# Kernel tuning notes

Measured on AMD Instinct MI355X. Metric: run time of the kernel, lower is better.

Reference implementation:

```python
import jax, jax.numpy as jnp
import numpy as np

B, T, D, E, TOP_K = 4, 4096, 1024, 8, 2
CAPACITY_FACTOR = 1.5


def setup_inputs() -> dict:
    key = jax.random.key(0)
    k1, k2, k3 = jax.random.split(key, 3)
    x = jax.random.normal(k1, (B, T, D), dtype=jnp.float32)
    Wr = jax.random.normal(k2, (E, D), dtype=jnp.float32) * 0.02   # router weight [E, D]
    We = jax.random.normal(k3, (E, D, D), dtype=jnp.float32) * 0.02  # per-expert dense [E, D, D]
    return {"x": x, "Wr": Wr, "We": We}


def reference(x, Wr, We):
    Bb, Tt, Dd = x.shape
    Ee = Wr.shape[0]
    K = TOP_K
    C = int(Tt * K / Ee * CAPACITY_FACTOR) + 1  # max_tokens_per_expert

    # Router + fused top-k softmax (triton_topk_softmax semantics)
    logits = jnp.einsum('btd,ed->bte', x, Wr)                 # [B, T, E]
    top_vals, top_idx = jax.lax.top_k(logits, K)              # [B, T, K]
    w = jax.nn.softmax(top_vals, axis=-1)                     # [B, T, K]

    # Position of each (token, k) slot inside its expert's capacity buffer,
    # assigned in (t, k) order -- matches the sequential counter in _build_position_map.
    flat_e = top_idx.reshape(Bb, Tt * K)                      # [B, T*K]
    oh = jax.nn.one_hot(flat_e, Ee, dtype=jnp.int32)          # [B, T*K, E]
    pos_all = jnp.cumsum(oh, axis=1) - oh                     # count of earlier slots per expert
    pos = jnp.take_along_axis(pos_all, flat_e[..., None], axis=-1)[..., 0]  # [B, T*K]
    keep = pos < C                                            # capacity drop

    # Scatter tokens into [B, E, C, D] capacity buffers (triton_expert_scatter)
    b_idx = jnp.arange(Bb, dtype=jnp.int32)[:, None]
    dst = (b_idx * Ee + flat_e) * C + pos                     # flat buffer index
    dst = jnp.where(keep, dst, Bb * Ee * C).reshape(-1)       # out-of-range -> dropped
    x_rep = jnp.repeat(x, K, axis=1).reshape(-1, Dd)          # [B*T*K, D]
    buf = jnp.zeros((Bb * Ee * C, Dd), dtype=x.dtype).at[dst].add(x_rep, mode='drop')
    expert_in = buf.reshape(Bb, Ee, C, Dd)

    # expert_fn: per-expert dense layer (grouped GEMM)
    expert_out = jnp.einsum('becd,edf->becf', expert_in, We)  # [B, E, C, D]

    # Gather back + weighted combine (triton_expert_gather)
    gathered = jnp.take(expert_out.reshape(Bb * Ee * C, Dd), dst, axis=0,
                        mode='fill', fill_value=0.0)          # dropped slots -> 0
    gathered = gathered.reshape(Bb, Tt, K, Dd)
    out = jnp.einsum('btk,btkd->btd', w, gathered)            # [B, T, D]
    return out
```

## Files before the change

kernel.cpp:

```cpp
#include <hip/hip_runtime.h>
#include <hip/hip_bf16.h>
#include <math.h>

#define B_ 4
#define T_ 4096
#define D_ 1024
#define E_ 8
#define K_ 2
#define C_ 1537

typedef short bf16x8 __attribute__((ext_vector_type(8)));
typedef float f32x4 __attribute__((ext_vector_type(4)));

__device__ __forceinline__ unsigned short f2bf(float f) {
    union { float f; unsigned int u; } c; c.f = f;
    unsigned int u = c.u;
    unsigned int r = (u + 0x7fffu + ((u >> 16) & 1u)) >> 16;
    return (unsigned short)r;
}

__device__ __forceinline__ void gl2lds16(const unsigned short* g, unsigned short* l) {
    __builtin_amdgcn_global_load_lds(
        (const __attribute__((address_space(1))) unsigned int*)g,
        (__attribute__((address_space(3))) unsigned int*)l, 16, 0, 0);
}

__global__ __launch_bounds__(256) void router_kernel(
    const float* __restrict__ x, const float* __restrict__ Wr,
    unsigned short* __restrict__ xbf, int* __restrict__ top_e,
    float* __restrict__ wbuf) {
    __shared__ float wr_s[E_ * D_];
    int tid = threadIdx.x;
    const float4* wr4 = (const float4*)Wr;
    float4* wrs4 = (float4*)wr_s;
    for (int i = tid; i < E_ * D_ / 4; i += 256) wrs4[i] = wr4[i];
    __syncthreads();

    int wave = tid >> 6, lane = tid & 63;
    int token = blockIdx.x * 4 + wave;

    const float4* xr = (const float4*)(x + (size_t)token * D_) + lane * 4;
    float xs[16];
    #pragma unroll
    for (int i = 0; i < 4; i++) {
        float4 v = xr[i];
        xs[i * 4 + 0] = v.x; xs[i * 4 + 1] = v.y;
        xs[i * 4 + 2] = v.z; xs[i * 4 + 3] = v.w;
    }

    unsigned short xb[16];
    #pragma unroll
    for (int i = 0; i < 16; i++) xb[i] = f2bf(xs[i]);
    uint4* dst = (uint4*)(xbf + (size_t)token * D_ + lane * 16);
    dst[0] = ((uint4*)xb)[0];
    dst[1] = ((uint4*)xb)[1];

    double acc[E_];
    #pragma unroll
    for (int e = 0; e < E_; e++) {
        const float* wp = wr_s + e * D_ + lane * 16;
        double a = 0.0;
        #pragma unroll
        for (int i = 0; i < 16; i++) a += (double)xs[i] * (double)wp[i];
        acc[e] = a;
    }
    #pragma unroll
    for (int e = 0; e < E_; e++) {
        #pragma unroll
        for (int off = 32; off > 0; off >>= 1)
            acc[e] += __shfl_down(acc[e], off, 64);
    }

    if (lane == 0) {
        int e0 = 0; double v0 = acc[0];
        #pragma unroll
        for (int e = 1; e < E_; e++) if (acc[e] > v0) { v0 = acc[e]; e0 = e; }
        int e1 = -1; double v1 = -1.0e300;
        #pragma unroll
        for (int e = 0; e < E_; e++) if (e != e0 && acc[e] > v1) { v1 = acc[e]; e1 = e; }
        double ex = exp(v1 - v0);
        float w0 = (float)(1.0 / (1.0 + ex));
        float w1 = (float)(ex / (1.0 + ex));
        top_e[token * 2 + 0] = e0;
        top_e[token * 2 + 1] = e1;
        wbuf[token * 2 + 0] = w0;
        wbuf[token * 2 + 1] = w1;
    }
}

__global__ __launch_bounds__(256) void wt_kernel(const float* __restrict__ We,
                                                 unsigned short* __restrict__ wtbf) {
    __shared__ unsigned short tile[64][65];
    int e = blockIdx.x >> 8;
    int t = blockIdx.x & 255;
    int d0 = (t >> 4) * 64, f0 = (t & 15) * 64;
    const float* src = We + ((size_t)e * D_ + d0) * D_ + f0;
    int tid = threadIdx.x;
    #pragma unroll
    for (int i = 0; i < 4; i++) {
        int idx = tid + i * 256;
        int r = idx >> 4, c4 = (idx & 15) * 4;
        float4 v = *(const float4*)(src + (size_t)r * D_ + c4);
        tile[r][c4 + 0] = f2bf(v.x); tile[r][c4 + 1] = f2bf(v.y);
        tile[r][c4 + 2] = f2bf(v.z); tile[r][c4 + 3] = f2bf(v.w);
    }
    __syncthreads();
    unsigned short* dstp = wtbf + ((size_t)e * D_ + f0) * D_ + d0;
    int r = tid >> 2, c0 = (tid & 3) * 16;
    unsigned short vals[16];
    #pragma unroll
    for (int j = 0; j < 16; j++) vals[j] = tile[c0 + j][r];
    *(uint4*)(dstp + (size_t)r * D_ + c0)     = ((const uint4*)vals)[0];
    *(uint4*)(dstp + (size_t)r * D_ + c0 + 8) = ((const uint4*)vals)[1];
}

__global__ __launch_bounds__(256) void scan_kernel(const int* __restrict__ top_e,
                                                   int* __restrict__ list,
                                                   int* __restrict__ count) {
    int b = blockIdx.x, tid = threadIdx.x;
    const int S = T_ * K_;
    const int per = S / 256;
    __shared__ int cnt[256][E_];
    int local[E_];
    #pragma unroll
    for (int e = 0; e < E_; e++) local[e] = 0;
    const int* te = top_e + (size_t)b * S + tid * per;
    int evals[32];
    for (int i = 0; i < per; i++) { evals[i] = te[i]; local[evals[i]]++; }
    #pragma unroll
    for (int e = 0; e < E_; e++) cnt[tid][e] = local[e];
    __syncthreads();
    if (tid < E_) {
        int run = 0;
        for (int i = 0; i < 256; i++) { int v = cnt[i][tid]; cnt[i][tid] = run; run += v; }
        count[b * E_ + tid] = min(run, C_);
    }
    __syncthreads();
    int base[E_];
    #pragma unroll
    for (int e = 0; e < E_; e++) base[e] = cnt[tid][e];
    int* lst = list + (size_t)b * E_ * C_;
    for (int i = 0; i < per; i++) {
        int ev = evals[i];
        int p = base[ev]++;
        if (p < C_) lst[ev * C_ + p] = tid * per + i;
    }
}

__global__ __launch_bounds__(256) void gemm_kernel(
    const unsigned short* __restrict__ xbf, const unsigned short* __restrict__ wtbf,
    const int* __restrict__ list, const int* __restrict__ count,
    const float* __restrict__ wbuf, float* __restrict__ out) {
    int cb = blockIdx.x & 7;
    int rb = (blockIdx.x >> 3) % 13;
    int pe = blockIdx.x / 104;
    int b = pe >> 3, e = pe & 7;
    int cnt = count[pe];
    int row0 = rb * 128;
    if (row0 >= cnt) return;
    int rows = min(128, cnt - row0);

    __shared__ unsigned short As[2][128 * 32];
    __shared__ unsigned short Bs[2][128 * 32];
    __shared__ int slots[128];

    int tid = threadIdx.x;
    if (tid < 128) slots[tid] = (tid < rows) ? list[pe * C_ + row0 + tid] : 0;
    __syncthreads();

    int w = tid >> 6, l = tid & 63;
    int rA0 = w * 16 + (l >> 2);
    int rA1 = rA0 + 64;
    int ch  = l & 3;
    int cS0 = ch ^ ((rA0 >> 1) & 3);
    int cS1 = ch ^ ((rA1 >> 1) & 3);
    int tA0 = slots[rA0] >> 1, tA1 = slots[rA1] >> 1;
    const unsigned short* gA0 = xbf + ((size_t)b * T_ + tA0) * D_ + cS0 * 8;
    const unsigned short* gA1 = xbf + ((size_t)b * T_ + tA1) * D_ + cS1 * 8;
    const unsigned short* gB0 = wtbf + ((size_t)e * D_ + cb * 128 + rA0) * D_ + cS0 * 8;
    const unsigned short* gB1 = wtbf + ((size_t)e * D_ + cb * 128 + rA1) * D_ + cS1 * 8;
    int sOff = w * 512 + l * 8;

    int wave = w, lane = l;
    int wm = wave >> 1, wn = wave & 1;
    int quad = lane >> 4, mrow = lane & 15;
    int qe = quad ^ ((mrow >> 1) & 3);
    int aRd = wm * 2048 + mrow * 32 + qe * 8;
    int bRd = wn * 2048 + mrow * 32 + qe * 8;

    f32x4 acc[4][4];
    #pragma unroll
    for (int i = 0; i < 4; i++)
        #pragma unroll
        for (int j = 0; j < 4; j++) acc[i][j] = (f32x4){0.f, 0.f, 0.f, 0.f};

#define STAGE(buf, kk) do {                                   \
        unsigned short* sA = &As[buf][sOff];                  \
        unsigned short* sB = &Bs[buf][sOff];                  \
        gl2lds16(gA0 + (kk) * 32, sA);                        \
        gl2lds16(gA1 + (kk) * 32, sA + 2048);                 \
        gl2lds16(gB0 + (kk) * 32, sB);                        \
        gl2lds16(gB1 + (kk) * 32, sB + 2048);                 \
    } while (0)

    STAGE(0, 0);
    __syncthreads();
    int cur = 0;
    for (int kk = 0; kk < 32; kk++) {
        if (kk < 31) STAGE(cur ^ 1, kk + 1);
        bf16x8 af[4], bfv[4];
        #pragma unroll
        for (int i = 0; i < 4; i++)
            af[i] = *(const bf16x8*)(&As[cur][aRd + i * 512]);
        #pragma unroll
        for (int j = 0; j < 4; j++)
            bfv[j] = *(const bf16x8*)(&Bs[cur][bRd + j * 512]);
        #pragma unroll
        for (int i = 0; i < 4; i++)
            #pragma unroll
            for (int j = 0; j < 4; j++)
                acc[i][j] = __builtin_amdgcn_mfma_f32_16x16x32_bf16(af[i], bfv[j], acc[i][j], 0, 0, 0);
        __syncthreads();
        cur ^= 1;
    }
#undef STAGE

    float* outb = out + (size_t)b * T_ * D_;
    const float* wb = wbuf + (size_t)b * T_ * 2;
    int ncolbase = cb * 128 + wn * 64 + mrow;
    #pragma unroll
    for (int i = 0; i < 4; i++) {
        #pragma unroll
        for (int r = 0; r < 4; r++) {
            int m = wm * 64 + i * 16 + quad * 4 + r;
            if (m < rows) {
                int s = slots[m];
                int t = s >> 1;
                float wgt = wb[t * 2 + (s & 1)];
                float* orow = outb + (size_t)t * D_;
                #pragma unroll
                for (int j = 0; j < 4; j++)
                    atomicAdd(orow + ncolbase + j * 16, wgt * acc[i][j][r]);
            }
        }
    }
}

extern "C" void kernel_launch(void* const* d_in, const int* in_sizes, int n_in,
                              void* d_out, int out_size, void* d_ws, size_t ws_size,
                              hipStream_t stream) {
    const float* x  = (const float*)d_in[0];
    const float* Wr = (const float*)d_in[1];
    const float* We = (const float*)d_in[2];
    float* out = (float*)d_out;
    char* ws = (char*)d_ws;

    unsigned short* xbf  = (unsigned short*)(ws);
    unsigned short* wtbf = (unsigned short*)(ws + 33554432);
    int*   top_e = (int*)  (ws + 50331648);
    float* wbuf  = (float*)(ws + 50462720);
    int*   list  = (int*)  (ws + 50593792);
    int*   count = (int*)  (ws + 50790528);

    hipMemsetAsync(d_out, 0, (size_t)out_size * sizeof(float), stream);
    router_kernel<<<dim3(B_ * T_ / 4), dim3(256), 0, stream>>>(x, Wr, xbf, top_e, wbuf);
    wt_kernel<<<dim3(E_ * 256), dim3(256), 0, stream>>>(We, wtbf);
    scan_kernel<<<dim3(B_), dim3(256), 0, stream>>>(top_e, list, count);
    gemm_kernel<<<dim3(32 * 13 * 8), dim3(256), 0, stream>>>(xbf, wtbf, list, count, wbuf, out);
}
```

Baseline: 348.7 us.

## Replace atomic combine with per-slot expert output buffer and combine kernel

After: 311.5 us. 1.12x faster.

```diff
diff --git a/kernel.cpp b/kernel.cpp
--- a/kernel.cpp
+++ b/kernel.cpp
@@ -116,7 +116,8 @@
 
 __global__ __launch_bounds__(256) void scan_kernel(const int* __restrict__ top_e,
                                                    int* __restrict__ list,
-                                                   int* __restrict__ count) {
+                                                   int* __restrict__ count,
+                                                   unsigned char* __restrict__ keep) {
     int b = blockIdx.x, tid = threadIdx.x;
     const int S = T_ * K_;
     const int per = S / 256;
@@ -140,17 +141,21 @@
     #pragma unroll
     for (int e = 0; e < E_; e++) base[e] = cnt[tid][e];
     int* lst = list + (size_t)b * E_ * C_;
+    unsigned char* kp = keep + (size_t)b * S + tid * per;
     for (int i = 0; i < per; i++) {
         int ev = evals[i];
         int p = base[ev]++;
-        if (p < C_) lst[ev * C_ + p] = tid * per + i;
+        int kept = (p < C_);
+        if (kept) lst[ev * C_ + p] = tid * per + i;
+        kp[i] = (unsigned char)kept;
     }
 }
 
 __global__ __launch_bounds__(256) void gemm_kernel(
     const unsigned short* __restrict__ xbf, const unsigned short* __restrict__ wtbf,
     const int* __restrict__ list, const int* __restrict__ count,
-    const float* __restrict__ wbuf, float* __restrict__ out) {
+    const float* __restrict__ wbuf, float* __restrict__ out,
+    float* __restrict__ eout) {
     int cb = blockIdx.x & 7;
     int rb = (blockIdx.x >> 3) % 13;
     int pe = blockIdx.x / 104;
@@ -225,25 +230,85 @@
     }
 #undef STAGE
 
-    float* outb = out + (size_t)b * T_ * D_;
-    const float* wb = wbuf + (size_t)b * T_ * 2;
     int ncolbase = cb * 128 + wn * 64 + mrow;
-    #pragma unroll
-    for (int i = 0; i < 4; i++) {
-        #pragma unroll
-        for (int r = 0; r < 4; r++) {
-            int m = wm * 64 + i * 16 + quad * 4 + r;
-            if (m < rows) {
-                int s = slots[m];
-                int t = s >> 1;
-                float wgt = wb[t * 2 + (s & 1)];
-                float* orow = outb + (size_t)t * D_;
-                #pragma unroll
-                for (int j = 0; j < 4; j++)
-                    atomicAdd(orow + ncolbase + j * 16, wgt * acc[i][j][r]);
+    if (eout != nullptr) {
+        float* ebase = eout + ((size_t)b * (T_ * K_)) * D_;
+        #pragma unroll
+        for (int i = 0; i < 4; i++) {
+            #pragma unroll
+            for (int r = 0; r < 4; r++) {
+                int m = wm * 64 + i * 16 + quad * 4 + r;
+                if (m < rows) {
+                    int s = slots[m];
+                    float* erow = ebase + (size_t)s * D_;
+                    #pragma unroll
+                    for (int j = 0; j < 4; j++)
+                        erow[ncolbase + j * 16] = acc[i][j][r];
+                }
             }
         }
-    }
+    } else {
+        float* outb = out + (size_t)b * T_ * D_;
+        const float* wb = wbuf + (size_t)b * T_ * 2;
+        #pragma unroll
+        for (int i = 0; i < 4; i++) {
+            #pragma unroll
+            for (int r = 0; r < 4; r++) {
+                int m = wm * 64 + i * 16 + quad * 4 + r;
+                if (m < rows) {
+                    int s = slots[m];
+                    int t = s >> 1;
+                    float wgt = wb[t * 2 + (s & 1)];
+                    float* orow = outb + (size_t)t * D_;
+                    #pragma unroll
+                    for (int j = 0; j < 4; j++)
+                        atomicAdd(orow + ncolbase + j * 16, wgt * acc[i][j][r]);
+                }
+            }
+        }
+    }
+}
+
+__global__ __launch_bounds__(256) void combine_kernel(
+    const float* __restrict__ eout, const float* __restrict__ wbuf,
+    const unsigned char* __restrict__ keep, float* __restrict__ out) {
+    int tid = threadIdx.x;
+    int wave = tid >> 6, lane = tid & 63;
+    int tok = blockIdx.x * 4 + wave;
+    int b = tok >> 12;
+    int tl = tok & (T_ - 1);
+    size_t slot0 = (size_t)b * (T_ * K_) + (size_t)tl * 2;
+
+    float w0 = wbuf[tok * 2 + 0];
+    float w1 = wbuf[tok * 2 + 1];
+    bool k0 = keep[slot0] != 0;
+    bool k1 = keep[slot0 + 1] != 0;
+
+    const float4* r0 = (const float4*)(eout + slot0 * D_) + lane * 4;
+    const float4* r1 = (const float4*)(eout + (slot0 + 1) * D_) + lane * 4;
+    float4* o = (float4*)(out + (size_t)tok * D_) + lane * 4;
+
+    float4 acc[4];
+    #pragma unroll
+    for (int i = 0; i < 4; i++) acc[i] = make_float4(0.f, 0.f, 0.f, 0.f);
+    if (k0) {
+        #pragma unroll
+        for (int i = 0; i < 4; i++) {
+            float4 v = r0[i];
+            acc[i].x += w0 * v.x; acc[i].y += w0 * v.y;
+            acc[i].z += w0 * v.z; acc[i].w += w0 * v.w;
+        }
+    }
+    if (k1) {
+        #pragma unroll
+        for (int i = 0; i < 4; i++) {
+            float4 v = r1[i];
+            acc[i].x += w1 * v.x; acc[i].y += w1 * v.y;
+            acc[i].z += w1 * v.z; acc[i].w += w1 * v.w;
+        }
+    }
+    #pragma unroll
+    for (int i = 0; i < 4; i++) o[i] = acc[i];
 }
 
 extern "C" void kernel_launch(void* const* d_in, const int* in_sizes, int n_in,
@@ -261,10 +326,20 @@
     float* wbuf  = (float*)(ws + 50462720);
     int*   list  = (int*)  (ws + 50593792);
     int*   count = (int*)  (ws + 50790528);
-
-    hipMemsetAsync(d_out, 0, (size_t)out_size * sizeof(float), stream);
+    unsigned char* keep = (unsigned char*)(ws + 50790656);
+    const size_t EOUT_OFF = 50823424ull;
+    float* eout = (float*)(ws + EOUT_OFF);
+    const size_t NEEDED = EOUT_OFF + (size_t)B_ * T_ * K_ * D_ * 4;
+
+    bool store_path = (ws_size >= NEEDED);
+
+    if (!store_path)
+        hipMemsetAsync(d_out, 0, (size_t)out_size * sizeof(float), stream);
     router_kernel<<<dim3(B_ * T_ / 4), dim3(256), 0, stream>>>(x, Wr, xbf, top_e, wbuf);
     wt_kernel<<<dim3(E_ * 256), dim3(256), 0, stream>>>(We, wtbf);
-    scan_kernel<<<dim3(B_), dim3(256), 0, stream>>>(top_e, list, count);
-    gemm_kernel<<<dim3(32 * 13 * 8), dim3(256), 0, stream>>>(xbf, wtbf, list, count, wbuf, out);
-}
+    scan_kernel<<<dim3(B_), dim3(256), 0, stream>>>(top_e, list, count, keep);
+    gemm_kernel<<<dim3(32 * 13 * 8), dim3(256), 0, stream>>>(
+        xbf, wtbf, list, count, wbuf, out, store_path ? eout : (float*)nullptr);
+    if (store_path)
+        combine_kernel<<<dim3(B_ * T_ / 4), dim3(256), 0, stream>>>(eout, wbuf, keep, out);
+}
```
